# Performance work log

Hardware: AMD Instinct MI355X
Metric: run time of the kernel (lower is better)

The kernel has to match this reference:

```python
import jax, jax.numpy as jnp
import numpy as np

EMB = 768
HS = 64
B, T = 4, 4096


def setup_inputs() -> dict:
    key = jax.random.key(0)
    ks = jax.random.split(key, 7)
    s = 1.0 / np.sqrt(EMB)
    return {
        "x": jax.random.normal(ks[0], (B, T, EMB), dtype=jnp.float32),
        "Wk": jax.random.normal(ks[1], (EMB, HS), dtype=jnp.float32) * s,
        "bk": jnp.zeros((HS,), dtype=jnp.float32),
        "Wq": jax.random.normal(ks[2], (EMB, HS), dtype=jnp.float32) * s,
        "bq": jnp.zeros((HS,), dtype=jnp.float32),
        "Wv": jax.random.normal(ks[3], (EMB, HS), dtype=jnp.float32) * s,
        "bv": jnp.zeros((HS,), dtype=jnp.float32),
    }


def reference(x, Wk, bk, Wq, bq, Wv, bv):
    # Linear projections: (B, T, emb) @ (emb, hs) + bias -> (B, T, hs)
    k = x @ Wk + bk
    q = x @ Wq + bq
    v = x @ Wv + bv
    # NOTE: original code computes key @ query^T (k on the left), no 1/sqrt(hs) scaling.
    att = jnp.einsum("bth,bsh->bts", k, q)  # (B, T, T)
    causal = jnp.tril(jnp.ones((T, T), dtype=bool))  # (T, T)
    att = jnp.where(causal, att, -jnp.inf)
    wei = jax.nn.softmax(att, axis=-1)
    return jnp.einsum("bts,bsh->bth", wei, v)  # (B, T, hs)
```

## Files before the change

kernel.cpp:

```cpp
#include <hip/hip_runtime.h>
#include <cmath>

static constexpr int EMB  = 768;
static constexpr int HS   = 64;
static constexpr int NB   = 4;
static constexpr int SEQ  = 4096;
static constexpr int MTOT = NB * SEQ;
static constexpr int SPLITS = 8;

typedef __attribute__((ext_vector_type(8))) short  short8x;
typedef __attribute__((ext_vector_type(4))) float  float4x;
typedef __attribute__((ext_vector_type(4))) unsigned short ushort4x;

__device__ inline unsigned short rne16(float f) {
    unsigned u = __builtin_bit_cast(unsigned, f);
    unsigned r = u + 0x7FFFu + ((u >> 16) & 1u);
    return (unsigned short)(r >> 16);
}
__device__ inline float bf2f(unsigned short h) {
    return __builtin_bit_cast(float, ((unsigned)h) << 16);
}

__global__ __launch_bounds__(256) void convert_w(
    const float* __restrict__ Wk, const float* __restrict__ Wq, const float* __restrict__ Wv,
    unsigned short* __restrict__ wpk)
{
    const int t    = blockIdx.x * 256 + threadIdx.x;
    const int lane = t & 63;
    const int rest = t >> 6;
    const int nng  = rest % 12;
    const int kcp  = rest / 12;
    const int kc   = kcp % 24;
    const int p    = kcp / 24;
    const int which= nng >> 2;
    const int nn   = nng & 3;
    const float* W = (which == 0) ? Wk : (which == 1) ? Wq : Wv;
    const int col  = nn * 16 + (lane & 15);
    const int kr   = kc * 32 + (lane >> 4) * 8;

    unsigned short o[8];
    #pragma unroll
    for (int j = 0; j < 8; ++j) {
        float w = W[(size_t)(kr + j) * HS + col];
        unsigned short h = rne16(w);
        o[j] = (p == 0) ? h : rne16(w - bf2f(h));
    }
    size_t base = ((size_t)((p * 24 + kc) * 12 + nng) * 64 + lane) * 8;
    *(short8x*)&wpk[base] = *(short8x*)o;
}

__global__ __launch_bounds__(256) void proj_kernel(
    const float* __restrict__ x,
    const unsigned short* __restrict__ wpk,
    const float* __restrict__ bk, const float* __restrict__ bq, const float* __restrict__ bv,
    unsigned short* __restrict__ khi, unsigned short* __restrict__ klo,
    unsigned short* __restrict__ qhi, unsigned short* __restrict__ qlo,
    unsigned short* __restrict__ vT)
{
    __shared__ unsigned short xh[2][32 * 72];
    __shared__ unsigned short xl[2][32 * 72];

    const int tid  = threadIdx.x;
    const int lane = tid & 63;
    const int w    = tid >> 6;
    const int l15  = lane & 15;
    const int quad = lane >> 4;
    const int row0 = blockIdx.x * 32;

    float4x acc[3][2] = {};
    float4  pre[2];

    #pragma unroll
    for (int it = 0; it < 2; ++it) {
        const int fi = tid + it * 256;
        const int r  = fi >> 4, c4 = (fi & 15) * 4;
        pre[it] = *(const float4*)&x[(size_t)(row0 + r) * EMB + 0 * 64 + c4];
    }
    #pragma unroll
    for (int it = 0; it < 2; ++it) {
        const int fi = tid + it * 256;
        const int r  = fi >> 4, c4 = (fi & 15) * 4;
        const float4 xv = pre[it];
        const unsigned short h0 = rne16(xv.x), h1 = rne16(xv.y),
                             h2 = rne16(xv.z), h3 = rne16(xv.w);
        ushort4x hv = {h0, h1, h2, h3};
        ushort4x lv = {rne16(xv.x - bf2f(h0)), rne16(xv.y - bf2f(h1)),
                       rne16(xv.z - bf2f(h2)), rne16(xv.w - bf2f(h3))};
        *(ushort4x*)&xh[0][r * 72 + c4] = hv;
        *(ushort4x*)&xl[0][r * 72 + c4] = lv;
    }

    for (int ch = 0; ch < 12; ++ch) {
        if (ch + 1 < 12) {
            #pragma unroll
            for (int it = 0; it < 2; ++it) {
                const int fi = tid + it * 256;
                const int r  = fi >> 4, c4 = (fi & 15) * 4;
                pre[it] = *(const float4*)&x[(size_t)(row0 + r) * EMB + (ch + 1) * 64 + c4];
            }
        }
        __syncthreads();
        const int buf = ch & 1;

        #pragma unroll
        for (int k0i = 0; k0i < 2; ++k0i) {
            const int k0 = k0i * 32;
            const int kc = ch * 2 + k0i;
            short8x ah[2], al[2];
            #pragma unroll
            for (int mi = 0; mi < 2; ++mi) {
                ah[mi] = *(const short8x*)&xh[buf][(mi * 16 + l15) * 72 + k0 + quad * 8];
                al[mi] = *(const short8x*)&xl[buf][(mi * 16 + l15) * 72 + k0 + quad * 8];
            }
            #pragma unroll
            for (int which = 0; which < 3; ++which) {
                const int nng = which * 4 + w;
                const short8x bh = *(const short8x*)&wpk[((size_t)((0 * 24 + kc) * 12 + nng) * 64 + lane) * 8];
                const short8x bl = *(const short8x*)&wpk[((size_t)((1 * 24 + kc) * 12 + nng) * 64 + lane) * 8];
                #pragma unroll
                for (int mi = 0; mi < 2; ++mi) {
                    acc[which][mi] = __builtin_amdgcn_mfma_f32_16x16x32_bf16(ah[mi], bh, acc[which][mi], 0, 0, 0);
                    acc[which][mi] = __builtin_amdgcn_mfma_f32_16x16x32_bf16(ah[mi], bl, acc[which][mi], 0, 0, 0);
                    acc[which][mi] = __builtin_amdgcn_mfma_f32_16x16x32_bf16(al[mi], bh, acc[which][mi], 0, 0, 0);
                }
            }
        }

        if (ch + 1 < 12) {
            const int nbuf = (ch + 1) & 1;
            #pragma unroll
            for (int it = 0; it < 2; ++it) {
                const int fi = tid + it * 256;
                const int r  = fi >> 4, c4 = (fi & 15) * 4;
                const float4 xv = pre[it];
                const unsigned short h0 = rne16(xv.x), h1 = rne16(xv.y),
                                     h2 = rne16(xv.z), h3 = rne16(xv.w);
                ushort4x hv = {h0, h1, h2, h3};
                ushort4x lv = {rne16(xv.x - bf2f(h0)), rne16(xv.y - bf2f(h1)),
                               rne16(xv.z - bf2f(h2)), rne16(xv.w - bf2f(h3))};
                *(ushort4x*)&xh[nbuf][r * 72 + c4] = hv;
                *(ushort4x*)&xl[nbuf][r * 72 + c4] = lv;
            }
        }
    }

    const int col = w * 16 + l15;
    const float bkv = bk[col], bqv = bq[col], bvv = bv[col];
    #pragma unroll
    for (int mi = 0; mi < 2; ++mi) {
        const int rbase = row0 + mi * 16 + quad * 4;
        #pragma unroll
        for (int r = 0; r < 4; ++r) {
            const float kv = acc[0][mi][r] + bkv;
            const unsigned short hk = rne16(kv);
            khi[(size_t)(rbase + r) * 64 + col] = hk;
            klo[(size_t)(rbase + r) * 64 + col] = rne16(kv - bf2f(hk));
            const float qv = acc[1][mi][r] + bqv;
            const unsigned short hq = rne16(qv);
            qhi[(size_t)(rbase + r) * 64 + col] = hq;
            qlo[(size_t)(rbase + r) * 64 + col] = rne16(qv - bf2f(hq));
        }
        const int b = rbase / SEQ;
        const int s = rbase % SEQ;
        ushort4x vv = {rne16(acc[2][mi][0] + bvv), rne16(acc[2][mi][1] + bvv),
                       rne16(acc[2][mi][2] + bvv), rne16(acc[2][mi][3] + bvv)};
        *(ushort4x*)&vT[((size_t)b * 64 + col) * SEQ + s] = vv;
    }
}

__global__ __launch_bounds__(256, 2) void attn_kernel(
    const unsigned short* __restrict__ khi, const unsigned short* __restrict__ klo,
    const unsigned short* __restrict__ qhi, const unsigned short* __restrict__ qlo,
    const unsigned short* __restrict__ vT,
    float* __restrict__ Opart, float* __restrict__ lpart)
{
    __shared__ unsigned short qh_s[64 * 72];
    __shared__ unsigned short ql_s[64 * 72];
    __shared__ unsigned short vt_s[64 * 72];
    __shared__ unsigned short psH[64 * 72];
    __shared__ unsigned short psL[64 * 72];

    const int tid  = threadIdx.x;
    const int lane = tid & 63;
    const int w    = tid >> 6;
    const int l15  = lane & 15;
    const int quad = lane >> 4;

    const int n  = blockIdx.x;
    const int sp = n & (SPLITS - 1);
    const int b  = (n >> 3) & (NB - 1);
    const int p  = n >> 5;
    const int jj[4] = {63 - p, 32 + p, 31 - p, p};
    const size_t rowb = (size_t)b * SEQ;

    float4x oacc[4][4] = {};
    float   l_r[4][4]  = {};

    const int sr = tid >> 3;
    const int c8 = (tid & 7) * 8;

    for (int ci = sp; ci <= jj[0]; ci += SPLITS) {
        const int s0 = ci * 64;
        __syncthreads();
        #pragma unroll
        for (int it = 0; it < 2; ++it) {
            const int r = sr + it * 32;
            *(short8x*)&qh_s[r * 72 + c8] = *(const short8x*)&qhi[(rowb + s0 + r) * 64 + c8];
            *(short8x*)&ql_s[r * 72 + c8] = *(const short8x*)&qlo[(rowb + s0 + r) * 64 + c8];
            *(short8x*)&vt_s[r * 72 + c8] = *(const short8x*)&vT[((size_t)b * 64 + r) * SEQ + s0 + c8];
        }
        __syncthreads();

        #pragma unroll
        for (int g = 0; g < 2; ++g) {
            const int idxH = g ? 1 : 0;
            const int idxL = g ? 2 : 3;
            const int jH = jj[idxH], jL = jj[idxL];
            const bool aH = (ci <= jH), aL = (ci <= jL);
            if (!aH && !aL) continue;

            short8x ahH[2], alH[2], ahL[2], alL[2];
            #pragma unroll
            for (int k0 = 0; k0 < 2; ++k0) {
                if (aH) {
                    const size_t rH = (rowb + jH * 64 + 16 * w + l15) * 64 + k0 * 32 + quad * 8;
                    ahH[k0] = *(const short8x*)&khi[rH];
                    alH[k0] = *(const short8x*)&klo[rH];
                }
                if (aL) {
                    const size_t rL = (rowb + jL * 64 + 16 * w + l15) * 64 + k0 * 32 + quad * 8;
                    ahL[k0] = *(const short8x*)&khi[rL];
                    alL[k0] = *(const short8x*)&klo[rL];
                }
            }

            float4x sH[4] = {}, sL[4] = {};
            __builtin_amdgcn_s_setprio(1);
            #pragma unroll
            for (int k0 = 0; k0 < 2; ++k0) {
                #pragma unroll
                for (int nn = 0; nn < 4; ++nn) {
                    const short8x bh = *(const short8x*)&qh_s[(nn * 16 + l15) * 72 + k0 * 32 + quad * 8];
                    const short8x bl = *(const short8x*)&ql_s[(nn * 16 + l15) * 72 + k0 * 32 + quad * 8];
                    if (aH) {
                        sH[nn] = __builtin_amdgcn_mfma_f32_16x16x32_bf16(ahH[k0], bh, sH[nn], 0, 0, 0);
                        sH[nn] = __builtin_amdgcn_mfma_f32_16x16x32_bf16(alH[k0], bh, sH[nn], 0, 0, 0);
                        sH[nn] = __builtin_amdgcn_mfma_f32_16x16x32_bf16(ahH[k0], bl, sH[nn], 0, 0, 0);
                    }
                    if (aL) {
                        sL[nn] = __builtin_amdgcn_mfma_f32_16x16x32_bf16(ahL[k0], bh, sL[nn], 0, 0, 0);
                        sL[nn] = __builtin_amdgcn_mfma_f32_16x16x32_bf16(alL[k0], bh, sL[nn], 0, 0, 0);
                        sL[nn] = __builtin_amdgcn_mfma_f32_16x16x32_bf16(ahL[k0], bl, sL[nn], 0, 0, 0);
                    }
                }
            }
            __builtin_amdgcn_s_setprio(0);

            #pragma unroll
            for (int hl = 0; hl < 2; ++hl) {
                const bool alive = hl ? aL : aH;
                if (!alive) continue;
                const int j   = hl ? jL : jH;
                const int idx = hl ? idxL : idxH;
                float4x* sc   = hl ? sL : sH;
                unsigned short* ps = hl ? psL : psH;
                if (ci == j) {
                    const int trow = j * 64 + 16 * w + quad * 4;
                    #pragma unroll
                    for (int nn = 0; nn < 4; ++nn) {
                        const int colg = s0 + nn * 16 + l15;
                        #pragma unroll
                        for (int r = 0; r < 4; ++r)
                            if (colg > trow + r) sc[nn][r] = -1e30f;
                    }
                }
                #pragma unroll
                for (int nn = 0; nn < 4; ++nn) {
                    #pragma unroll
                    for (int r = 0; r < 4; ++r) {
                        const float e = __expf(fminf(sc[nn][r], 80.0f));
                        const unsigned short h = rne16(e);
                        l_r[idx][r] += bf2f(h);
                        ps[(16 * w + quad * 4 + r) * 72 + nn * 16 + l15] = h;
                    }
                }
            }

            __builtin_amdgcn_s_setprio(1);
            #pragma unroll
            for (int k0 = 0; k0 < 2; ++k0) {
                short8x paH, paL;
                if (aH) paH = *(const short8x*)&psH[(16 * w + l15) * 72 + k0 * 32 + quad * 8];
                if (aL) paL = *(const short8x*)&psL[(16 * w + l15) * 72 + k0 * 32 + quad * 8];
                #pragma unroll
                for (int nn = 0; nn < 4; ++nn) {
                    const short8x vb = *(const short8x*)&vt_s[(nn * 16 + l15) * 72 + k0 * 32 + quad * 8];
                    if (aH) oacc[idxH][nn] = __builtin_amdgcn_mfma_f32_16x16x32_bf16(paH, vb, oacc[idxH][nn], 0, 0, 0);
                    if (aL) oacc[idxL][nn] = __builtin_amdgcn_mfma_f32_16x16x32_bf16(paL, vb, oacc[idxL][nn], 0, 0, 0);
                }
            }
            __builtin_amdgcn_s_setprio(0);
        }
    }

    #pragma unroll
    for (int idx = 0; idx < 4; ++idx) {
        const int j = jj[idx];
        if (idx == 3 && sp > p) continue;
        float lv[4];
        #pragma unroll
        for (int r = 0; r < 4; ++r) {
            float l = l_r[idx][r];
            l += __shfl_xor(l, 1);
            l += __shfl_xor(l, 2);
            l += __shfl_xor(l, 4);
            l += __shfl_xor(l, 8);
            lv[r] = l;
        }
        const size_t part = (size_t)(j * NB + b) * SPLITS + sp;
        float* Op = Opart + part * 4096;
        #pragma unroll
        for (int nn = 0; nn < 4; ++nn)
            #pragma unroll
            for (int r = 0; r < 4; ++r)
                Op[(16 * w + quad * 4 + r) * 64 + nn * 16 + l15] = oacc[idx][nn][r];
        if (l15 == 0) {
            #pragma unroll
            for (int r = 0; r < 4; ++r)
                lpart[part * 64 + 16 * w + quad * 4 + r] = lv[r];
        }
    }
}

__global__ __launch_bounds__(256) void combine_kernel(
    const float* __restrict__ Opart, const float* __restrict__ lpart,
    float* __restrict__ out)
{
    const int j   = blockIdx.x;
    const int b   = blockIdx.y;
    const int tid = threadIdx.x;
    const int row = tid >> 2;
    const int c0  = (tid & 3) * 16;
    const size_t base = (size_t)(j * NB + b) * SPLITS;

    float4 acc[4] = {};
    float lsum = 0.f;
    for (int sp = 0; sp < SPLITS; ++sp) {
        const float l = lpart[(base + sp) * 64 + row];
        if (l > 0.f) {
            lsum += l;
            const float* Op = Opart + (base + sp) * 4096 + row * 64 + c0;
            #pragma unroll
            for (int u = 0; u < 4; ++u) {
                const float4 v = *(const float4*)&Op[u * 4];
                acc[u].x += v.x; acc[u].y += v.y; acc[u].z += v.z; acc[u].w += v.w;
            }
        }
    }
    const float inv = 1.0f / lsum;
    float* o = out + ((size_t)b * SEQ + j * 64 + row) * 64 + c0;
    #pragma unroll
    for (int u = 0; u < 4; ++u) {
        float4 v;
        v.x = acc[u].x * inv; v.y = acc[u].y * inv;
        v.z = acc[u].z * inv; v.w = acc[u].w * inv;
        *(float4*)&o[u * 4] = v;
    }
}

extern "C" void kernel_launch(void* const* d_in, const int* in_sizes, int n_in,
                              void* d_out, int out_size, void* d_ws, size_t ws_size,
                              hipStream_t stream)
{
    const float* x  = (const float*)d_in[0];
    const float* Wk = (const float*)d_in[1];
    const float* bk = (const float*)d_in[2];
    const float* Wq = (const float*)d_in[3];
    const float* bq = (const float*)d_in[4];
    const float* Wv = (const float*)d_in[5];
    const float* bv = (const float*)d_in[6];
    float* out = (float*)d_out;

    const size_t NE = (size_t)MTOT * HS;
    unsigned short* khi = (unsigned short*)d_ws;
    unsigned short* klo = khi + NE;
    unsigned short* qhi = klo + NE;
    unsigned short* qlo = qhi + NE;
    unsigned short* vT  = qlo + NE;
    unsigned short* wpk = vT + NE;
    float* Opart = (float*)(wpk + 294912);
    float* lpart = Opart + (size_t)64 * NB * SPLITS * 4096;

    hipMemsetAsync(lpart, 0, (size_t)64 * NB * SPLITS * 64 * sizeof(float), stream);
    convert_w<<<144, 256, 0, stream>>>(Wk, Wq, Wv, wpk);
    proj_kernel<<<MTOT / 32, 256, 0, stream>>>(x, wpk, bk, bq, bv, khi, klo, qhi, qlo, vT);
    attn_kernel<<<16 * NB * SPLITS, 256, 0, stream>>>(khi, klo, qhi, qlo, vT, Opart, lpart);
    dim3 cgrid(64, NB);
    combine_kernel<<<cgrid, 256, 0, stream>>>(Opart, lpart, out);
}
```

Baseline: 161.9 us.

## Split attention blocks to two query tiles each and widen combine grid

Each attention block now owns two query tiles (one high, one low pair) instead of four, doubling the grid, shrinking accumulator registers and dropping one shared-memory P buffer. Launch bounds go from 2 to 4 blocks per SM to raise occupancy. The combine kernel is also split along rows over a third grid dimension, so each thread handles one float4. In exchange, each Q/V tile loaded into shared memory is now reused by two query tiles instead of four, so that traffic doubles, and the tighter register cap could cause spills.

```diff
diff --git a/kernel.cpp b/kernel.cpp
--- a/kernel.cpp
+++ b/kernel.cpp
@@ -168,7 +168,7 @@
     }
 }
 
-__global__ __launch_bounds__(256, 2) void attn_kernel(
+__global__ __launch_bounds__(256, 4) void attn_kernel(
     const unsigned short* __restrict__ khi, const unsigned short* __restrict__ klo,
     const unsigned short* __restrict__ qhi, const unsigned short* __restrict__ qlo,
     const unsigned short* __restrict__ vT,
@@ -177,8 +177,7 @@
     __shared__ unsigned short qh_s[64 * 72];
     __shared__ unsigned short ql_s[64 * 72];
     __shared__ unsigned short vt_s[64 * 72];
-    __shared__ unsigned short psH[64 * 72];
-    __shared__ unsigned short psL[64 * 72];
+    __shared__ unsigned short ps  [64 * 72];
 
     const int tid  = threadIdx.x;
     const int lane = tid & 63;
@@ -189,17 +188,20 @@
     const int n  = blockIdx.x;
     const int sp = n & (SPLITS - 1);
     const int b  = (n >> 3) & (NB - 1);
-    const int p  = n >> 5;
-    const int jj[4] = {63 - p, 32 + p, 31 - p, p};
+    const int ph = n >> 5;
+    const int p  = ph >> 1;
+    const int h  = ph & 1;
+    const int jH = h ? (32 + p) : (63 - p);
+    const int jL = h ? (31 - p) : p;
     const size_t rowb = (size_t)b * SEQ;
 
-    float4x oacc[4][4] = {};
-    float   l_r[4][4]  = {};
+    float4x oacc[2][4] = {};
+    float   l_r[2][4]  = {};
 
     const int sr = tid >> 3;
     const int c8 = (tid & 7) * 8;
 
-    for (int ci = sp; ci <= jj[0]; ci += SPLITS) {
+    for (int ci = sp; ci <= jH; ci += SPLITS) {
         const int s0 = ci * 64;
         __syncthreads();
         #pragma unroll
@@ -211,92 +213,76 @@
         }
         __syncthreads();
 
-        #pragma unroll
-        for (int g = 0; g < 2; ++g) {
-            const int idxH = g ? 1 : 0;
-            const int idxL = g ? 2 : 3;
-            const int jH = jj[idxH], jL = jj[idxL];
-            const bool aH = (ci <= jH), aL = (ci <= jL);
-            if (!aH && !aL) continue;
-
-            short8x ahH[2], alH[2], ahL[2], alL[2];
-            #pragma unroll
-            for (int k0 = 0; k0 < 2; ++k0) {
-                if (aH) {
-                    const size_t rH = (rowb + jH * 64 + 16 * w + l15) * 64 + k0 * 32 + quad * 8;
-                    ahH[k0] = *(const short8x*)&khi[rH];
-                    alH[k0] = *(const short8x*)&klo[rH];
-                }
+        const bool aL = (ci <= jL);
+
+        short8x ahH[2], alH[2], ahL[2], alL[2];
+        #pragma unroll
+        for (int k0 = 0; k0 < 2; ++k0) {
+            const size_t rH = (rowb + jH * 64 + 16 * w + l15) * 64 + k0 * 32 + quad * 8;
+            ahH[k0] = *(const short8x*)&khi[rH];
+            alH[k0] = *(const short8x*)&klo[rH];
+            if (aL) {
+                const size_t rL = (rowb + jL * 64 + 16 * w + l15) * 64 + k0 * 32 + quad * 8;
+                ahL[k0] = *(const short8x*)&khi[rL];
+                alL[k0] = *(const short8x*)&klo[rL];
+            }
+        }
+
+        float4x sH[4] = {}, sL[4] = {};
+        __builtin_amdgcn_s_setprio(1);
+        #pragma unroll
+        for (int k0 = 0; k0 < 2; ++k0) {
+            #pragma unroll
+            for (int nn = 0; nn < 4; ++nn) {
+                const short8x bh = *(const short8x*)&qh_s[(nn * 16 + l15) * 72 + k0 * 32 + quad * 8];
+                const short8x bl = *(const short8x*)&ql_s[(nn * 16 + l15) * 72 + k0 * 32 + quad * 8];
+                sH[nn] = __builtin_amdgcn_mfma_f32_16x16x32_bf16(ahH[k0], bh, sH[nn], 0, 0, 0);
+                sH[nn] = __builtin_amdgcn_mfma_f32_16x16x32_bf16(alH[k0], bh, sH[nn], 0, 0, 0);
+                sH[nn] = __builtin_amdgcn_mfma_f32_16x16x32_bf16(ahH[k0], bl, sH[nn], 0, 0, 0);
                 if (aL) {
-                    const size_t rL = (rowb + jL * 64 + 16 * w + l15) * 64 + k0 * 32 + quad * 8;
-                    ahL[k0] = *(const short8x*)&khi[rL];
-                    alL[k0] = *(const short8x*)&klo[rL];
-                }
-            }
-
-            float4x sH[4] = {}, sL[4] = {};
-            __builtin_amdgcn_s_setprio(1);
-            #pragma unroll
-            for (int k0 = 0; k0 < 2; ++k0) {
+                    sL[nn] = __builtin_amdgcn_mfma_f32_16x16x32_bf16(ahL[k0], bh, sL[nn], 0, 0, 0);
+                    sL[nn] = __builtin_amdgcn_mfma_f32_16x16x32_bf16(alL[k0], bh, sL[nn], 0, 0, 0);
+                    sL[nn] = __builtin_amdgcn_mfma_f32_16x16x32_bf16(ahL[k0], bl, sL[nn], 0, 0, 0);
+                }
+            }
+        }
+        __builtin_amdgcn_s_setprio(0);
+
+        #pragma unroll
+        for (int hl = 0; hl < 2; ++hl) {
+            if (hl == 1 && !aL) continue;
+            const int j = hl ? jL : jH;
+            float4x* sc = hl ? sL : sH;
+
+            if (ci == j) {
+                const int trow = j * 64 + 16 * w + quad * 4;
                 #pragma unroll
                 for (int nn = 0; nn < 4; ++nn) {
-                    const short8x bh = *(const short8x*)&qh_s[(nn * 16 + l15) * 72 + k0 * 32 + quad * 8];
-                    const short8x bl = *(const short8x*)&ql_s[(nn * 16 + l15) * 72 + k0 * 32 + quad * 8];
-                    if (aH) {
-                        sH[nn] = __builtin_amdgcn_mfma_f32_16x16x32_bf16(ahH[k0], bh, sH[nn], 0, 0, 0);
-                        sH[nn] = __builtin_amdgcn_mfma_f32_16x16x32_bf16(alH[k0], bh, sH[nn], 0, 0, 0);
-                        sH[nn] = __builtin_amdgcn_mfma_f32_16x16x32_bf16(ahH[k0], bl, sH[nn], 0, 0, 0);
-                    }
-                    if (aL) {
-                        sL[nn] = __builtin_amdgcn_mfma_f32_16x16x32_bf16(ahL[k0], bh, sL[nn], 0, 0, 0);
-                        sL[nn] = __builtin_amdgcn_mfma_f32_16x16x32_bf16(alL[k0], bh, sL[nn], 0, 0, 0);
-                        sL[nn] = __builtin_amdgcn_mfma_f32_16x16x32_bf16(ahL[k0], bl, sL[nn], 0, 0, 0);
-                    }
-                }
-            }
-            __builtin_amdgcn_s_setprio(0);
-
-            #pragma unroll
-            for (int hl = 0; hl < 2; ++hl) {
-                const bool alive = hl ? aL : aH;
-                if (!alive) continue;
-                const int j   = hl ? jL : jH;
-                const int idx = hl ? idxL : idxH;
-                float4x* sc   = hl ? sL : sH;
-                unsigned short* ps = hl ? psL : psH;
-                if (ci == j) {
-                    const int trow = j * 64 + 16 * w + quad * 4;
+                    const int colg = s0 + nn * 16 + l15;
                     #pragma unroll
-                    for (int nn = 0; nn < 4; ++nn) {
-                        const int colg = s0 + nn * 16 + l15;
-                        #pragma unroll
-                        for (int r = 0; r < 4; ++r)
-                            if (colg > trow + r) sc[nn][r] = -1e30f;
-                    }
-                }
+                    for (int r = 0; r < 4; ++r)
+                        if (colg > trow + r) sc[nn][r] = -1e30f;
+                }
+            }
+            #pragma unroll
+            for (int nn = 0; nn < 4; ++nn) {
                 #pragma unroll
-                for (int nn = 0; nn < 4; ++nn) {
-                    #pragma unroll
-                    for (int r = 0; r < 4; ++r) {
-                        const float e = __expf(fminf(sc[nn][r], 80.0f));
-                        const unsigned short h = rne16(e);
-                        l_r[idx][r] += bf2f(h);
-                        ps[(16 * w + quad * 4 + r) * 72 + nn * 16 + l15] = h;
-                    }
+                for (int r = 0; r < 4; ++r) {
+                    const float e = __expf(fminf(sc[nn][r], 80.0f));
+                    const unsigned short hh = rne16(e);
+                    l_r[hl][r] += bf2f(hh);
+                    ps[(16 * w + quad * 4 + r) * 72 + nn * 16 + l15] = hh;
                 }
             }
 
             __builtin_amdgcn_s_setprio(1);
             #pragma unroll
             for (int k0 = 0; k0 < 2; ++k0) {
-                short8x paH, paL;
-                if (aH) paH = *(const short8x*)&psH[(16 * w + l15) * 72 + k0 * 32 + quad * 8];
-                if (aL) paL = *(const short8x*)&psL[(16 * w + l15) * 72 + k0 * 32 + quad * 8];
+                const short8x pa = *(const short8x*)&ps[(16 * w + l15) * 72 + k0 * 32 + quad * 8];
                 #pragma unroll
                 for (int nn = 0; nn < 4; ++nn) {
                     const short8x vb = *(const short8x*)&vt_s[(nn * 16 + l15) * 72 + k0 * 32 + quad * 8];
-                    if (aH) oacc[idxH][nn] = __builtin_amdgcn_mfma_f32_16x16x32_bf16(paH, vb, oacc[idxH][nn], 0, 0, 0);
-                    if (aL) oacc[idxL][nn] = __builtin_amdgcn_mfma_f32_16x16x32_bf16(paL, vb, oacc[idxL][nn], 0, 0, 0);
+                    oacc[hl][nn] = __builtin_amdgcn_mfma_f32_16x16x32_bf16(pa, vb, oacc[hl][nn], 0, 0, 0);
                 }
             }
             __builtin_amdgcn_s_setprio(0);
@@ -304,13 +290,13 @@
     }
 
     #pragma unroll
-    for (int idx = 0; idx < 4; ++idx) {
-        const int j = jj[idx];
-        if (idx == 3 && sp > p) continue;
+    for (int hl = 0; hl < 2; ++hl) {
+        const int j = hl ? jL : jH;
+        if (sp > j) continue;
         float lv[4];
         #pragma unroll
         for (int r = 0; r < 4; ++r) {
-            float l = l_r[idx][r];
+            float l = l_r[hl][r];
             l += __shfl_xor(l, 1);
             l += __shfl_xor(l, 2);
             l += __shfl_xor(l, 4);
@@ -323,7 +309,7 @@
         for (int nn = 0; nn < 4; ++nn)
             #pragma unroll
             for (int r = 0; r < 4; ++r)
-                Op[(16 * w + quad * 4 + r) * 64 + nn * 16 + l15] = oacc[idx][nn][r];
+                Op[(16 * w + quad * 4 + r) * 64 + nn * 16 + l15] = oacc[hl][nn][r];
         if (l15 == 0) {
             #pragma unroll
             for (int r = 0; r < 4; ++r)
@@ -339,33 +325,24 @@
     const int j   = blockIdx.x;
     const int b   = blockIdx.y;
     const int tid = threadIdx.x;
-    const int row = tid >> 2;
-    const int c0  = (tid & 3) * 16;
+    const int row = blockIdx.z * 16 + (tid >> 4);
+    const int c0  = (tid & 15) * 4;
     const size_t base = (size_t)(j * NB + b) * SPLITS;
 
-    float4 acc[4] = {};
+    float4 acc = {0.f, 0.f, 0.f, 0.f};
     float lsum = 0.f;
     for (int sp = 0; sp < SPLITS; ++sp) {
         const float l = lpart[(base + sp) * 64 + row];
         if (l > 0.f) {
             lsum += l;
-            const float* Op = Opart + (base + sp) * 4096 + row * 64 + c0;
-            #pragma unroll
-            for (int u = 0; u < 4; ++u) {
-                const float4 v = *(const float4*)&Op[u * 4];
-                acc[u].x += v.x; acc[u].y += v.y; acc[u].z += v.z; acc[u].w += v.w;
-            }
+            const float4 v = *(const float4*)&Opart[(base + sp) * 4096 + row * 64 + c0];
+            acc.x += v.x; acc.y += v.y; acc.z += v.z; acc.w += v.w;
         }
     }
     const float inv = 1.0f / lsum;
-    float* o = out + ((size_t)b * SEQ + j * 64 + row) * 64 + c0;
-    #pragma unroll
-    for (int u = 0; u < 4; ++u) {
-        float4 v;
-        v.x = acc[u].x * inv; v.y = acc[u].y * inv;
-        v.z = acc[u].z * inv; v.w = acc[u].w * inv;
-        *(float4*)&o[u * 4] = v;
-    }
+    float4 v;
+    v.x = acc.x * inv; v.y = acc.y * inv; v.z = acc.z * inv; v.w = acc.w * inv;
+    *(float4*)&out[((size_t)b * SEQ + j * 64 + row) * 64 + c0] = v;
 }
 
 extern "C" void kernel_launch(void* const* d_in, const int* in_sizes, int n_in,
@@ -394,7 +371,7 @@
     hipMemsetAsync(lpart, 0, (size_t)64 * NB * SPLITS * 64 * sizeof(float), stream);
     convert_w<<<144, 256, 0, stream>>>(Wk, Wq, Wv, wpk);
     proj_kernel<<<MTOT / 32, 256, 0, stream>>>(x, wpk, bk, bq, bv, khi, klo, qhi, qlo, vT);
-    attn_kernel<<<16 * NB * SPLITS, 256, 0, stream>>>(khi, klo, qhi, qlo, vT, Opart, lpart);
-    dim3 cgrid(64, NB);
+    attn_kernel<<<16 * NB * SPLITS * 2, 256, 0, stream>>>(khi, klo, qhi, qlo, vT, Opart, lpart);
+    dim3 cgrid(64, NB, 4);
     combine_kernel<<<cgrid, 256, 0, stream>>>(Opart, lpart, out);
 }
```

Result: slower. 172.2 us (+6.4%).

## Prefetch next Q/V tile into registers and hoist K loads; spread combine across more blocks

Applied to the files above, without the earlier changes.

The attention loop now loads the next iteration's Q-hi, Q-lo and V-transposed tile into registers while the current tile is being processed. It also hoists the K fragment loads for all four row blocks ahead of the barrier, so global latency overlaps the LDS stores and synchronisation. The combine kernel splits each 64-row tile across four z-blocks, with one float4 per thread, to raise parallelism. The cost is higher register pressure from holding 16 K fragments plus the prefetch buffers, which may lower occupancy or cause spills.

```diff
diff --git a/kernel.cpp b/kernel.cpp
--- a/kernel.cpp
+++ b/kernel.cpp
@@ -199,15 +199,53 @@
     const int sr = tid >> 3;
     const int c8 = (tid & 7) * 8;
 
+    short8x pq[2], pl[2], pv[2];
+    {
+        const int s0 = sp * 64;
+        #pragma unroll
+        for (int it = 0; it < 2; ++it) {
+            const int r = sr + it * 32;
+            pq[it] = *(const short8x*)&qhi[(rowb + s0 + r) * 64 + c8];
+            pl[it] = *(const short8x*)&qlo[(rowb + s0 + r) * 64 + c8];
+            pv[it] = *(const short8x*)&vT[((size_t)b * 64 + r) * SEQ + s0 + c8];
+        }
+    }
+
     for (int ci = sp; ci <= jj[0]; ci += SPLITS) {
         const int s0 = ci * 64;
+
+        short8x ah[4][2], al[4][2];
+        bool av[4];
+        #pragma unroll
+        for (int idx = 0; idx < 4; ++idx) {
+            av[idx] = (ci <= jj[idx]);
+            if (av[idx]) {
+                #pragma unroll
+                for (int k0 = 0; k0 < 2; ++k0) {
+                    const size_t rr = (rowb + jj[idx] * 64 + 16 * w + l15) * 64 + k0 * 32 + quad * 8;
+                    ah[idx][k0] = *(const short8x*)&khi[rr];
+                    al[idx][k0] = *(const short8x*)&klo[rr];
+                }
+            }
+        }
+
         __syncthreads();
         #pragma unroll
         for (int it = 0; it < 2; ++it) {
             const int r = sr + it * 32;
-            *(short8x*)&qh_s[r * 72 + c8] = *(const short8x*)&qhi[(rowb + s0 + r) * 64 + c8];
-            *(short8x*)&ql_s[r * 72 + c8] = *(const short8x*)&qlo[(rowb + s0 + r) * 64 + c8];
-            *(short8x*)&vt_s[r * 72 + c8] = *(const short8x*)&vT[((size_t)b * 64 + r) * SEQ + s0 + c8];
+            *(short8x*)&qh_s[r * 72 + c8] = pq[it];
+            *(short8x*)&ql_s[r * 72 + c8] = pl[it];
+            *(short8x*)&vt_s[r * 72 + c8] = pv[it];
+        }
+        if (ci + SPLITS <= jj[0]) {
+            const int s1 = (ci + SPLITS) * 64;
+            #pragma unroll
+            for (int it = 0; it < 2; ++it) {
+                const int r = sr + it * 32;
+                pq[it] = *(const short8x*)&qhi[(rowb + s1 + r) * 64 + c8];
+                pl[it] = *(const short8x*)&qlo[(rowb + s1 + r) * 64 + c8];
+                pv[it] = *(const short8x*)&vT[((size_t)b * 64 + r) * SEQ + s1 + c8];
+            }
         }
         __syncthreads();
 
@@ -216,23 +254,8 @@
             const int idxH = g ? 1 : 0;
             const int idxL = g ? 2 : 3;
             const int jH = jj[idxH], jL = jj[idxL];
-            const bool aH = (ci <= jH), aL = (ci <= jL);
+            const bool aH = av[idxH], aL = av[idxL];
             if (!aH && !aL) continue;
-
-            short8x ahH[2], alH[2], ahL[2], alL[2];
-            #pragma unroll
-            for (int k0 = 0; k0 < 2; ++k0) {
-                if (aH) {
-                    const size_t rH = (rowb + jH * 64 + 16 * w + l15) * 64 + k0 * 32 + quad * 8;
-                    ahH[k0] = *(const short8x*)&khi[rH];
-                    alH[k0] = *(const short8x*)&klo[rH];
-                }
-                if (aL) {
-                    const size_t rL = (rowb + jL * 64 + 16 * w + l15) * 64 + k0 * 32 + quad * 8;
-                    ahL[k0] = *(const short8x*)&khi[rL];
-                    alL[k0] = *(const short8x*)&klo[rL];
-                }
-            }
 
             float4x sH[4] = {}, sL[4] = {};
             __builtin_amdgcn_s_setprio(1);
@@ -243,14 +266,14 @@
                     const short8x bh = *(const short8x*)&qh_s[(nn * 16 + l15) * 72 + k0 * 32 + quad * 8];
                     const short8x bl = *(const short8x*)&ql_s[(nn * 16 + l15) * 72 + k0 * 32 + quad * 8];
                     if (aH) {
-                        sH[nn] = __builtin_amdgcn_mfma_f32_16x16x32_bf16(ahH[k0], bh, sH[nn], 0, 0, 0);
-                        sH[nn] = __builtin_amdgcn_mfma_f32_16x16x32_bf16(alH[k0], bh, sH[nn], 0, 0, 0);
-                        sH[nn] = __builtin_amdgcn_mfma_f32_16x16x32_bf16(ahH[k0], bl, sH[nn], 0, 0, 0);
+                        sH[nn] = __builtin_amdgcn_mfma_f32_16x16x32_bf16(ah[idxH][k0], bh, sH[nn], 0, 0, 0);
+                        sH[nn] = __builtin_amdgcn_mfma_f32_16x16x32_bf16(al[idxH][k0], bh, sH[nn], 0, 0, 0);
+                        sH[nn] = __builtin_amdgcn_mfma_f32_16x16x32_bf16(ah[idxH][k0], bl, sH[nn], 0, 0, 0);
                     }
                     if (aL) {
-                        sL[nn] = __builtin_amdgcn_mfma_f32_16x16x32_bf16(ahL[k0], bh, sL[nn], 0, 0, 0);
-                        sL[nn] = __builtin_amdgcn_mfma_f32_16x16x32_bf16(alL[k0], bh, sL[nn], 0, 0, 0);
-                        sL[nn] = __builtin_amdgcn_mfma_f32_16x16x32_bf16(ahL[k0], bl, sL[nn], 0, 0, 0);
+                        sL[nn] = __builtin_amdgcn_mfma_f32_16x16x32_bf16(ah[idxL][k0], bh, sL[nn], 0, 0, 0);
+                        sL[nn] = __builtin_amdgcn_mfma_f32_16x16x32_bf16(al[idxL][k0], bh, sL[nn], 0, 0, 0);
+                        sL[nn] = __builtin_amdgcn_mfma_f32_16x16x32_bf16(ah[idxL][k0], bl, sL[nn], 0, 0, 0);
                     }
                 }
             }
@@ -339,33 +362,24 @@
     const int j   = blockIdx.x;
     const int b   = blockIdx.y;
     const int tid = threadIdx.x;
-    const int row = tid >> 2;
-    const int c0  = (tid & 3) * 16;
+    const int row = blockIdx.z * 16 + (tid >> 4);
+    const int c0  = (tid & 15) * 4;
     const size_t base = (size_t)(j * NB + b) * SPLITS;
 
-    float4 acc[4] = {};
+    float4 acc = {0.f, 0.f, 0.f, 0.f};
     float lsum = 0.f;
     for (int sp = 0; sp < SPLITS; ++sp) {
         const float l = lpart[(base + sp) * 64 + row];
         if (l > 0.f) {
             lsum += l;
-            const float* Op = Opart + (base + sp) * 4096 + row * 64 + c0;
-            #pragma unroll
-            for (int u = 0; u < 4; ++u) {
-                const float4 v = *(const float4*)&Op[u * 4];
-                acc[u].x += v.x; acc[u].y += v.y; acc[u].z += v.z; acc[u].w += v.w;
-            }
+            const float4 v = *(const float4*)&Opart[(base + sp) * 4096 + row * 64 + c0];
+            acc.x += v.x; acc.y += v.y; acc.z += v.z; acc.w += v.w;
         }
     }
     const float inv = 1.0f / lsum;
-    float* o = out + ((size_t)b * SEQ + j * 64 + row) * 64 + c0;
-    #pragma unroll
-    for (int u = 0; u < 4; ++u) {
-        float4 v;
-        v.x = acc[u].x * inv; v.y = acc[u].y * inv;
-        v.z = acc[u].z * inv; v.w = acc[u].w * inv;
-        *(float4*)&o[u * 4] = v;
-    }
+    float4 v;
+    v.x = acc.x * inv; v.y = acc.y * inv; v.z = acc.z * inv; v.w = acc.w * inv;
+    *(float4*)&out[((size_t)b * SEQ + j * 64 + row) * 64 + c0] = v;
 }
 
 extern "C" void kernel_launch(void* const* d_in, const int* in_sizes, int n_in,
@@ -395,6 +409,6 @@
     convert_w<<<144, 256, 0, stream>>>(Wk, Wq, Wv, wpk);
     proj_kernel<<<MTOT / 32, 256, 0, stream>>>(x, wpk, bk, bq, bv, khi, klo, qhi, qlo, vT);
     attn_kernel<<<16 * NB * SPLITS, 256, 0, stream>>>(khi, klo, qhi, qlo, vT, Opart, lpart);
-    dim3 cgrid(64, NB);
+    dim3 cgrid(64, NB, 4);
     combine_kernel<<<cgrid, 256, 0, stream>>>(Opart, lpart, out);
 }
```

Measured after the change: 176.4 us. 1.09x slower.
